# Kernel tuning notes

Hardware: AMD Instinct MI355X
Metric: run time of the kernel (lower is better)

The kernel has to match this reference:

```python
import jax, jax.numpy as jnp
import numpy as np

N, T, D, H = 64, 1024, 512, 512

def setup_inputs() -> dict:
    key = jax.random.key(0)
    k1, k2, k3, k4 = jax.random.split(key, 4)
    x = jax.random.normal(k1, (N, T, D), dtype=jnp.float32)
    h0 = jax.random.normal(k2, (N, H), dtype=jnp.float32)
    Wx = jax.random.normal(k3, (D, H), dtype=jnp.float32) / jnp.sqrt(jnp.float32(D))
    Wh = jax.random.normal(k4, (H, H), dtype=jnp.float32) / jnp.sqrt(jnp.float32(H))
    b = jnp.zeros((H,), dtype=jnp.float32)
    return {"x": x, "h0": h0, "Wx": Wx, "Wh": Wh, "b": b}

def reference(x, h0, Wx, Wh, b):
    # Precompute input projection for all timesteps: (N,T,H)
    xW = jnp.einsum('ntd,dh->nth', x, Wx) + b
    # Sequential recurrence over time via lax.scan
    def step(prev_h, xw_t):
        next_h = jnp.tanh(prev_h @ Wh + xw_t)  # (N,H)
        return next_h, next_h
    # scan over time axis: move T to leading axis
    _, h_seq = jax.lax.scan(step, h0, jnp.swapaxes(xW, 0, 1))  # (T,N,H)
    return jnp.swapaxes(h_seq, 0, 1)  # (N,T,H)
```

## Files before the change

### kernel.cpp

```cpp
#include <hip/hip_runtime.h>
#include <hip/hip_fp16.h>
#include <cstddef>
#include <cstdint>

#define NB 64
#define TT 1024
#define DD 512
#define HH 512

typedef _Float16 h2_t __attribute__((ext_vector_type(2)));
typedef __attribute__((ext_vector_type(8))) short bf16x8;
typedef __attribute__((ext_vector_type(4))) float f32x4;
typedef __attribute__((ext_vector_type(8))) unsigned short ushort8;

__device__ __forceinline__ float dot2f(uint32_t a, uint32_t b, float c) {
#if __has_builtin(__builtin_amdgcn_fdot2)
    return __builtin_amdgcn_fdot2(__builtin_bit_cast(h2_t, a),
                                  __builtin_bit_cast(h2_t, b), c, false);
#else
    __half2 av = __builtin_bit_cast(__half2, a);
    __half2 bv = __builtin_bit_cast(__half2, b);
    float2 af = __half22float2(av), bf = __half22float2(bv);
    return fmaf(af.x, bf.x, fmaf(af.y, bf.y, c));
#endif
}

__device__ __forceinline__ float fast_tanh(float z) {
    z = fmaxf(-15.f, fminf(15.f, z));
    float u = __builtin_amdgcn_exp2f(-2.885390082f * z);
    return (1.f - u) * __builtin_amdgcn_rcpf(1.f + u);
}

__device__ __forceinline__ unsigned short f2bf(float f) {
    uint32_t u = __builtin_bit_cast(uint32_t, f);
    u += 0x7FFFu + ((u >> 16) & 1u);
    return (unsigned short)(u >> 16);
}

__global__ void conv_x(const float* __restrict__ x,
                       unsigned short* __restrict__ xb, long total) {
    long i0 = (long)(blockIdx.x * blockDim.x + threadIdx.x) * 8;
    long stride = (long)gridDim.x * blockDim.x * 8;
    for (long i = i0; i < total; i += stride) {
        float4 a = *reinterpret_cast<const float4*>(&x[i]);
        float4 b = *reinterpret_cast<const float4*>(&x[i + 4]);
        ushort8 o;
        o[0] = f2bf(a.x); o[1] = f2bf(a.y); o[2] = f2bf(a.z); o[3] = f2bf(a.w);
        o[4] = f2bf(b.x); o[5] = f2bf(b.y); o[6] = f2bf(b.z); o[7] = f2bf(b.w);
        *reinterpret_cast<ushort8*>(&xb[i]) = o;
    }
}

__global__ void conv_wt(const float* __restrict__ W,
                        unsigned short* __restrict__ Wt) {
    int n = blockIdx.x;
    int kc = threadIdx.x;
    ushort8 o;
#pragma unroll
    for (int i = 0; i < 8; ++i)
        o[i] = f2bf(W[(size_t)(kc * 8 + i) * HH + n]);
    *reinterpret_cast<ushort8*>(&Wt[(size_t)n * DD + kc * 8]) = o;
}

#define GBM 128
#define GBN 128
#define GBK 64
#define LDSW 72

__global__ __launch_bounds__(256, 4) void gemm_bf16(
    const unsigned short* __restrict__ A,
    const unsigned short* __restrict__ Bt,
    const float* __restrict__ bias,
    float* __restrict__ C)
{
    __shared__ unsigned short As[GBM * LDSW];
    __shared__ unsigned short Bs[GBN * LDSW];

    const int tid  = threadIdx.x;
    const int m0   = blockIdx.x * GBM;
    const int n0   = blockIdx.y * GBN;
    const int lane = tid & 63;
    const int wave = tid >> 6;
    const int wm   = wave >> 1;
    const int wn   = wave & 1;

    const int srow = tid >> 3;
    const int sch  = tid & 7;

    f32x4 acc[4][4] = {};

    const int arow = wm * 64 + (lane & 15);
    const int brow = wn * 64 + (lane & 15);
    const int koff = (lane >> 4) * 8;

    for (int kt = 0; kt < DD / GBK; ++kt) {
        const int k0 = kt * GBK;
#pragma unroll
        for (int p = 0; p < 4; ++p) {
            const int row = srow + p * 32;
            *reinterpret_cast<ushort8*>(&As[row * LDSW + sch * 8]) =
                *reinterpret_cast<const ushort8*>(
                    &A[(size_t)(m0 + row) * DD + k0 + sch * 8]);
            *reinterpret_cast<ushort8*>(&Bs[row * LDSW + sch * 8]) =
                *reinterpret_cast<const ushort8*>(
                    &Bt[(size_t)(n0 + row) * DD + k0 + sch * 8]);
        }
        __syncthreads();

#pragma unroll
        for (int kk = 0; kk < GBK; kk += 32) {
            bf16x8 af[4], bf[4];
#pragma unroll
            for (int mt = 0; mt < 4; ++mt)
                af[mt] = *reinterpret_cast<const bf16x8*>(
                    &As[(arow + mt * 16) * LDSW + kk + koff]);
#pragma unroll
            for (int nt = 0; nt < 4; ++nt)
                bf[nt] = *reinterpret_cast<const bf16x8*>(
                    &Bs[(brow + nt * 16) * LDSW + kk + koff]);
#pragma unroll
            for (int mt = 0; mt < 4; ++mt)
#pragma unroll
                for (int nt = 0; nt < 4; ++nt)
                    acc[mt][nt] = __builtin_amdgcn_mfma_f32_16x16x32_bf16(
                        af[mt], bf[nt], acc[mt][nt], 0, 0, 0);
        }
        __syncthreads();
    }

#pragma unroll
    for (int nt = 0; nt < 4; ++nt) {
        const int col = n0 + wn * 64 + nt * 16 + (lane & 15);
        const float bv = bias[col];
#pragma unroll
        for (int mt = 0; mt < 4; ++mt) {
            const int rbase = m0 + wm * 64 + mt * 16 + (lane >> 4) * 4;
#pragma unroll
            for (int r = 0; r < 4; ++r)
                C[(size_t)(rbase + r) * HH + col] = acc[mt][nt][r] + bv;
        }
    }
}

#define BM 128
#define BN 128
#define BK 8

__global__ __launch_bounds__(256, 2) void gemm_xw(
    const float* __restrict__ A,
    const float* __restrict__ B,
    const float* __restrict__ bias,
    float* __restrict__ C)
{
    __shared__ float As[BK][BM];
    __shared__ float Bs[BK][BN];

    const int tid  = threadIdx.x;
    const int tm   = tid >> 4;
    const int tn   = tid & 15;
    const int row0 = blockIdx.x * BM;
    const int col0 = blockIdx.y * BN;

    const int ar = tid >> 1;
    const int ac = (tid & 1) * 4;
    const int br = tid >> 5;
    const int bc = (tid & 31) * 4;

    float acc[8][8];
#pragma unroll
    for (int i = 0; i < 8; ++i)
#pragma unroll
        for (int j = 0; j < 8; ++j) acc[i][j] = 0.f;

    for (int k0 = 0; k0 < DD; k0 += BK) {
        float4 av = *reinterpret_cast<const float4*>(
            &A[(size_t)(row0 + ar) * DD + k0 + ac]);
        float4 bv = *reinterpret_cast<const float4*>(
            &B[(size_t)(k0 + br) * HH + col0 + bc]);

        As[ac + 0][ar] = av.x;
        As[ac + 1][ar] = av.y;
        As[ac + 2][ar] = av.z;
        As[ac + 3][ar] = av.w;
        *reinterpret_cast<float4*>(&Bs[br][bc]) = bv;
        __syncthreads();

#pragma unroll
        for (int kk = 0; kk < BK; ++kk) {
            float a[8], b[8];
            *reinterpret_cast<float4*>(&a[0]) =
                *reinterpret_cast<const float4*>(&As[kk][tm * 8]);
            *reinterpret_cast<float4*>(&a[4]) =
                *reinterpret_cast<const float4*>(&As[kk][tm * 8 + 4]);
            *reinterpret_cast<float4*>(&b[0]) =
                *reinterpret_cast<const float4*>(&Bs[kk][tn * 8]);
            *reinterpret_cast<float4*>(&b[4]) =
                *reinterpret_cast<const float4*>(&Bs[kk][tn * 8 + 4]);
#pragma unroll
            for (int i = 0; i < 8; ++i)
#pragma unroll
                for (int j = 0; j < 8; ++j)
                    acc[i][j] = fmaf(a[i], b[j], acc[i][j]);
        }
        __syncthreads();
    }

#pragma unroll
    for (int i = 0; i < 8; ++i) {
        const int row = row0 + tm * 8 + i;
#pragma unroll
        for (int j = 0; j < 8; j += 4) {
            const int col = col0 + tn * 8 + j;
            float4 o;
            o.x = acc[i][j + 0] + bias[col + 0];
            o.y = acc[i][j + 1] + bias[col + 1];
            o.z = acc[i][j + 2] + bias[col + 2];
            o.w = acc[i][j + 3] + bias[col + 3];
            *reinterpret_cast<float4*>(&C[(size_t)row * HH + col]) = o;
        }
    }
}

__global__ __launch_bounds__(1024, 4) void rnn_scan_pkt(
    const float* __restrict__ Wh,
    const float* __restrict__ h0,
    float* __restrict__ out,
    uint64_t* __restrict__ exch)
{
    __shared__ __align__(16) uint32_t hp[2][HH / 2];
    __shared__ float partial[16][128];

    const int blk = blockIdx.x;
    const int x = blk & 7;
    const int i = blk >> 3;
    const int n = x + ((i & 7) << 3);
    const int r = i >> 3;
    const int jb = r << 7;

    const int tid = threadIdx.x;
    const int w = tid >> 6;
    const int l = tid & 63;

    uint32_t w0[16], w1[16];
    {
        const float* wc = Wh + (size_t)(w * 32) * HH + jb + l;
#pragma unroll
        for (int p = 0; p < 16; ++p) {
            float e0 = wc[(size_t)(2 * p) * HH];
            float e1 = wc[(size_t)(2 * p + 1) * HH];
            w0[p] = __builtin_bit_cast(uint32_t, __floats2half2_rn(e0, e1));
            float f0 = wc[(size_t)(2 * p) * HH + 64];
            float f1 = wc[(size_t)(2 * p + 1) * HH + 64];
            w1[p] = __builtin_bit_cast(uint32_t, __floats2half2_rn(f0, f1));
        }
    }

    if (tid < HH)
        ((__half*)hp[0])[tid] = __float2half(h0[(size_t)n * HH + tid]);
    __syncthreads();

    float* outn = out + (size_t)n * TT * HH;
    uint64_t* ex = exch + (size_t)n * 2 * HH;

    const int rcol = (jb + 128 + (tid - 128)) & (HH - 1);

    int cur = 0;
    for (int t = 0; t < TT; ++t) {
        const uint32_t T = (uint32_t)(t + 1);
        const int slot = (int)(T & 1u);

        float xw_r = 0.f;
        if (tid < 128) xw_r = outn[(size_t)t * HH + jb + tid];

        const uint32_t* hpw = &hp[cur][w * 16];
        float a0 = 0.f, a1 = 0.f, b0 = 0.f, b1 = 0.f;
#pragma unroll
        for (int q = 0; q < 4; ++q) {
            uint4 hv = ((const uint4*)hpw)[q];
            a0 = dot2f(hv.x, w0[4 * q + 0], a0);
            b0 = dot2f(hv.x, w1[4 * q + 0], b0);
            a1 = dot2f(hv.y, w0[4 * q + 1], a1);
            b1 = dot2f(hv.y, w1[4 * q + 1], b1);
            a0 = dot2f(hv.z, w0[4 * q + 2], a0);
            b0 = dot2f(hv.z, w1[4 * q + 2], b0);
            a1 = dot2f(hv.w, w0[4 * q + 3], a1);
            b1 = dot2f(hv.w, w1[4 * q + 3], b1);
        }
        partial[w][l] = a0 + a1;
        partial[w][64 + l] = b0 + b1;
        __syncthreads();

        __half* hpn = (__half*)hp[cur ^ 1];
        if (tid < 128) {
            float s = 0.f;
#pragma unroll
            for (int ww = 0; ww < 16; ++ww) s += partial[ww][tid];
            float h = fast_tanh(s + xw_r);
            outn[(size_t)t * HH + jb + tid] = h;
            hpn[jb + tid] = __float2half(h);
            uint64_t pk = ((uint64_t)T << 32) |
                          (uint64_t)__builtin_bit_cast(uint32_t, h);
            __hip_atomic_store(&ex[slot * HH + jb + tid], pk,
                               __ATOMIC_RELAXED, __HIP_MEMORY_SCOPE_AGENT);
        } else if (tid < 512) {
            uint64_t pk = __hip_atomic_load(&ex[slot * HH + rcol],
                                            __ATOMIC_RELAXED,
                                            __HIP_MEMORY_SCOPE_AGENT);
            while ((uint32_t)(pk >> 32) != T) {
                __builtin_amdgcn_s_sleep(1);
                pk = __hip_atomic_load(&ex[slot * HH + rcol],
                                       __ATOMIC_RELAXED,
                                       __HIP_MEMORY_SCOPE_AGENT);
            }
            hpn[rcol] = __float2half(__builtin_bit_cast(float, (uint32_t)pk));
        }
        __syncthreads();
        cur ^= 1;
    }
}

__global__ __launch_bounds__(512, 2) void rnn_scan_f32(
    const float* __restrict__ Wh,
    const float* __restrict__ h0,
    float* __restrict__ out)
{
    __shared__ float hbuf[2][HH];
    const int n = blockIdx.x;
    const int j = threadIdx.x;

    hbuf[0][j] = h0[(size_t)n * HH + j];
    __syncthreads();

    float* outn = out + (size_t)n * TT * HH;
    const float* __restrict__ wp = Wh + j;

    int cur = 0;
    for (int t = 0; t < TT; ++t) {
        float acc = outn[(size_t)t * HH + j];
        const float* hc = hbuf[cur];
#pragma unroll 4
        for (int k = 0; k < HH; k += 4) {
            float4 hv = *reinterpret_cast<const float4*>(&hc[k]);
            acc = fmaf(hv.x, wp[(size_t)(k + 0) * HH], acc);
            acc = fmaf(hv.y, wp[(size_t)(k + 1) * HH], acc);
            acc = fmaf(hv.z, wp[(size_t)(k + 2) * HH], acc);
            acc = fmaf(hv.w, wp[(size_t)(k + 3) * HH], acc);
        }
        float hn = tanhf(acc);
        outn[(size_t)t * HH + j] = hn;
        hbuf[cur ^ 1][j] = hn;
        cur ^= 1;
        __syncthreads();
    }
}

extern "C" void kernel_launch(void* const* d_in, const int* in_sizes, int n_in,
                              void* d_out, int out_size, void* d_ws, size_t ws_size,
                              hipStream_t stream) {
    const float* x  = (const float*)d_in[0];
    const float* h0 = (const float*)d_in[1];
    const float* Wx = (const float*)d_in[2];
    const float* Wh = (const float*)d_in[3];
    const float* b  = (const float*)d_in[4];
    float* out = (float*)d_out;

    const long   M        = (long)NB * TT;
    const size_t exch_b   = (size_t)NB * 2 * HH * 8;
    const size_t wt_b     = (size_t)HH * DD * 2;
    const size_t xb_b     = (size_t)M * DD * 2;
    const size_t need_mid = exch_b;
    const size_t need_all = exch_b + wt_b + xb_b;

    if (ws_size >= need_all) {
        uint64_t*       exch = (uint64_t*)d_ws;
        unsigned short* Wt   = (unsigned short*)((char*)d_ws + exch_b);
        unsigned short* xb   = (unsigned short*)((char*)d_ws + exch_b + wt_b);

        conv_x<<<2048, 256, 0, stream>>>(x, xb, M * DD);
        conv_wt<<<HH, 64, 0, stream>>>(Wx, Wt);
        dim3 gg(M / GBM, HH / GBN);
        gemm_bf16<<<gg, 256, 0, stream>>>(xb, Wt, b, out);
        rnn_scan_pkt<<<256, 1024, 0, stream>>>(Wh, h0, out, exch);
    } else if (ws_size >= need_mid) {
        dim3 g1(M / BM, HH / BN);
        gemm_xw<<<g1, 256, 0, stream>>>(x, Wx, b, out);
        rnn_scan_pkt<<<256, 1024, 0, stream>>>(Wh, h0, out, (uint64_t*)d_ws);
    } else {
        dim3 g1(M / BM, HH / BN);
        gemm_xw<<<g1, 256, 0, stream>>>(x, Wx, b, out);
        rnn_scan_f32<<<NB, 512, 0, stream>>>(Wh, h0, out);
    }
}
```

Measured before the change: 1.471 ms.

## Fuse bf16 conversion into GEMM and run recurrence in one block per sequence

```diff
diff --git a/kernel.cpp b/kernel.cpp
--- a/kernel.cpp
+++ b/kernel.cpp
@@ -7,6 +7,8 @@
 #define TT 1024
 #define DD 512
 #define HH 512
+#define WREG 92
+#define WLDS 36
 
 typedef _Float16 h2_t __attribute__((ext_vector_type(2)));
 typedef __attribute__((ext_vector_type(8))) short bf16x8;
@@ -37,20 +39,6 @@
     return (unsigned short)(u >> 16);
 }
 
-__global__ void conv_x(const float* __restrict__ x,
-                       unsigned short* __restrict__ xb, long total) {
-    long i0 = (long)(blockIdx.x * blockDim.x + threadIdx.x) * 8;
-    long stride = (long)gridDim.x * blockDim.x * 8;
-    for (long i = i0; i < total; i += stride) {
-        float4 a = *reinterpret_cast<const float4*>(&x[i]);
-        float4 b = *reinterpret_cast<const float4*>(&x[i + 4]);
-        ushort8 o;
-        o[0] = f2bf(a.x); o[1] = f2bf(a.y); o[2] = f2bf(a.z); o[3] = f2bf(a.w);
-        o[4] = f2bf(b.x); o[5] = f2bf(b.y); o[6] = f2bf(b.z); o[7] = f2bf(b.w);
-        *reinterpret_cast<ushort8*>(&xb[i]) = o;
-    }
-}
-
 __global__ void conv_wt(const float* __restrict__ W,
                         unsigned short* __restrict__ Wt) {
     int n = blockIdx.x;
@@ -67,8 +55,8 @@
 #define GBK 64
 #define LDSW 72
 
-__global__ __launch_bounds__(256, 4) void gemm_bf16(
-    const unsigned short* __restrict__ A,
+__global__ __launch_bounds__(256, 4) void gemm_bf16f(
+    const float* __restrict__ X,
     const unsigned short* __restrict__ Bt,
     const float* __restrict__ bias,
     float* __restrict__ C)
@@ -84,6 +72,8 @@
     const int wm   = wave >> 1;
     const int wn   = wave & 1;
 
+    const int axr = tid >> 1;
+    const int axc = (tid & 1) * 32;
     const int srow = tid >> 3;
     const int sch  = tid & 7;
 
@@ -95,12 +85,23 @@
 
     for (int kt = 0; kt < DD / GBK; ++kt) {
         const int k0 = kt * GBK;
+        {
+            const float* xp = &X[(size_t)(m0 + axr) * DD + k0 + axc];
+#pragma unroll
+            for (int i = 0; i < 4; ++i) {
+                float4 a = *reinterpret_cast<const float4*>(&xp[i * 8]);
+                float4 b = *reinterpret_cast<const float4*>(&xp[i * 8 + 4]);
+                ushort8 o;
+                o[0] = f2bf(a.x); o[1] = f2bf(a.y);
+                o[2] = f2bf(a.z); o[3] = f2bf(a.w);
+                o[4] = f2bf(b.x); o[5] = f2bf(b.y);
+                o[6] = f2bf(b.z); o[7] = f2bf(b.w);
+                *reinterpret_cast<ushort8*>(&As[axr * LDSW + axc + i * 8]) = o;
+            }
+        }
 #pragma unroll
         for (int p = 0; p < 4; ++p) {
             const int row = srow + p * 32;
-            *reinterpret_cast<ushort8*>(&As[row * LDSW + sch * 8]) =
-                *reinterpret_cast<const ushort8*>(
-                    &A[(size_t)(m0 + row) * DD + k0 + sch * 8]);
             *reinterpret_cast<ushort8*>(&Bs[row * LDSW + sch * 8]) =
                 *reinterpret_cast<const ushort8*>(
                     &Bt[(size_t)(n0 + row) * DD + k0 + sch * 8]);
@@ -221,136 +222,84 @@
     }
 }
 
-__global__ __launch_bounds__(1024, 4) void rnn_scan_pkt(
-    const float* __restrict__ Wh,
-    const float* __restrict__ h0,
-    float* __restrict__ out,
-    uint64_t* __restrict__ exch)
-{
-    __shared__ __align__(16) uint32_t hp[2][HH / 2];
-    __shared__ float partial[16][128];
-
-    const int blk = blockIdx.x;
-    const int x = blk & 7;
-    const int i = blk >> 3;
-    const int n = x + ((i & 7) << 3);
-    const int r = i >> 3;
-    const int jb = r << 7;
-
-    const int tid = threadIdx.x;
-    const int w = tid >> 6;
-    const int l = tid & 63;
-
-    uint32_t w0[16], w1[16];
-    {
-        const float* wc = Wh + (size_t)(w * 32) * HH + jb + l;
-#pragma unroll
-        for (int p = 0; p < 16; ++p) {
-            float e0 = wc[(size_t)(2 * p) * HH];
-            float e1 = wc[(size_t)(2 * p + 1) * HH];
-            w0[p] = __builtin_bit_cast(uint32_t, __floats2half2_rn(e0, e1));
-            float f0 = wc[(size_t)(2 * p) * HH + 64];
-            float f1 = wc[(size_t)(2 * p + 1) * HH + 64];
-            w1[p] = __builtin_bit_cast(uint32_t, __floats2half2_rn(f0, f1));
-        }
-    }
-
-    if (tid < HH)
-        ((__half*)hp[0])[tid] = __float2half(h0[(size_t)n * HH + tid]);
-    __syncthreads();
-
-    float* outn = out + (size_t)n * TT * HH;
-    uint64_t* ex = exch + (size_t)n * 2 * HH;
-
-    const int rcol = (jb + 128 + (tid - 128)) & (HH - 1);
-
-    int cur = 0;
-    for (int t = 0; t < TT; ++t) {
-        const uint32_t T = (uint32_t)(t + 1);
-        const int slot = (int)(T & 1u);
-
-        float xw_r = 0.f;
-        if (tid < 128) xw_r = outn[(size_t)t * HH + jb + tid];
-
-        const uint32_t* hpw = &hp[cur][w * 16];
-        float a0 = 0.f, a1 = 0.f, b0 = 0.f, b1 = 0.f;
-#pragma unroll
-        for (int q = 0; q < 4; ++q) {
-            uint4 hv = ((const uint4*)hpw)[q];
-            a0 = dot2f(hv.x, w0[4 * q + 0], a0);
-            b0 = dot2f(hv.x, w1[4 * q + 0], b0);
-            a1 = dot2f(hv.y, w0[4 * q + 1], a1);
-            b1 = dot2f(hv.y, w1[4 * q + 1], b1);
-            a0 = dot2f(hv.z, w0[4 * q + 2], a0);
-            b0 = dot2f(hv.z, w1[4 * q + 2], b0);
-            a1 = dot2f(hv.w, w0[4 * q + 3], a1);
-            b1 = dot2f(hv.w, w1[4 * q + 3], b1);
-        }
-        partial[w][l] = a0 + a1;
-        partial[w][64 + l] = b0 + b1;
-        __syncthreads();
-
-        __half* hpn = (__half*)hp[cur ^ 1];
-        if (tid < 128) {
-            float s = 0.f;
-#pragma unroll
-            for (int ww = 0; ww < 16; ++ww) s += partial[ww][tid];
-            float h = fast_tanh(s + xw_r);
-            outn[(size_t)t * HH + jb + tid] = h;
-            hpn[jb + tid] = __float2half(h);
-            uint64_t pk = ((uint64_t)T << 32) |
-                          (uint64_t)__builtin_bit_cast(uint32_t, h);
-            __hip_atomic_store(&ex[slot * HH + jb + tid], pk,
-                               __ATOMIC_RELAXED, __HIP_MEMORY_SCOPE_AGENT);
-        } else if (tid < 512) {
-            uint64_t pk = __hip_atomic_load(&ex[slot * HH + rcol],
-                                            __ATOMIC_RELAXED,
-                                            __HIP_MEMORY_SCOPE_AGENT);
-            while ((uint32_t)(pk >> 32) != T) {
-                __builtin_amdgcn_s_sleep(1);
-                pk = __hip_atomic_load(&ex[slot * HH + rcol],
-                                       __ATOMIC_RELAXED,
-                                       __HIP_MEMORY_SCOPE_AGENT);
-            }
-            hpn[rcol] = __float2half(__builtin_bit_cast(float, (uint32_t)pk));
-        }
-        __syncthreads();
-        cur ^= 1;
-    }
-}
-
-__global__ __launch_bounds__(512, 2) void rnn_scan_f32(
+__global__ __launch_bounds__(1024, 4) void rnn_scan_reg(
     const float* __restrict__ Wh,
     const float* __restrict__ h0,
     float* __restrict__ out)
 {
-    __shared__ float hbuf[2][HH];
-    const int n = blockIdx.x;
-    const int j = threadIdx.x;
-
-    hbuf[0][j] = h0[(size_t)n * HH + j];
+    __shared__ uint32_t Wl[2][9][HH][4];
+    __shared__ __align__(16) uint32_t hp[2][HH / 2];
+    __shared__ float partial[2][HH];
+
+    const int tid  = threadIdx.x;
+    const int j    = tid & (HH - 1);
+    const int half = tid >> 9;
+    const int n    = blockIdx.x;
+
+    uint32_t w[WREG];
+    {
+        const float* wc = Wh + (size_t)(half * 256) * HH + j;
+#pragma unroll
+        for (int p = 0; p < WREG; ++p) {
+            float e0 = wc[(size_t)(2 * p) * HH];
+            float e1 = wc[(size_t)(2 * p + 1) * HH];
+            w[p] = __builtin_bit_cast(uint32_t, __floats2half2_rn(e0, e1));
+        }
+    }
+    for (int idx = tid; idx < 2 * 9 * 4 * HH; idx += 1024) {
+        int jj  = idx & (HH - 1);
+        int e   = (idx >> 9) & 3;
+        int rem = idx >> 11;
+        int lg  = rem % 9;
+        int hf  = rem / 9;
+        int k2  = hf * 128 + WREG + 4 * lg + e;
+        float e0 = Wh[(size_t)(2 * k2) * HH + jj];
+        float e1 = Wh[(size_t)(2 * k2 + 1) * HH + jj];
+        Wl[hf][lg][jj][e] =
+            __builtin_bit_cast(uint32_t, __floats2half2_rn(e0, e1));
+    }
+
+    if (tid < HH)
+        ((__half*)hp[0])[tid] = __float2half(h0[(size_t)n * HH + tid]);
     __syncthreads();
 
     float* outn = out + (size_t)n * TT * HH;
-    const float* __restrict__ wp = Wh + j;
 
     int cur = 0;
     for (int t = 0; t < TT; ++t) {
-        float acc = outn[(size_t)t * HH + j];
-        const float* hc = hbuf[cur];
-#pragma unroll 4
-        for (int k = 0; k < HH; k += 4) {
-            float4 hv = *reinterpret_cast<const float4*>(&hc[k]);
-            acc = fmaf(hv.x, wp[(size_t)(k + 0) * HH], acc);
-            acc = fmaf(hv.y, wp[(size_t)(k + 1) * HH], acc);
-            acc = fmaf(hv.z, wp[(size_t)(k + 2) * HH], acc);
-            acc = fmaf(hv.w, wp[(size_t)(k + 3) * HH], acc);
-        }
-        float hn = tanhf(acc);
-        outn[(size_t)t * HH + j] = hn;
-        hbuf[cur ^ 1][j] = hn;
+        float xw = 0.f;
+        if (tid < HH) xw = outn[(size_t)t * HH + tid];
+
+        const uint4* hpw = (const uint4*)&hp[cur][half * 128];
+        float a0 = 0.f, a1 = 0.f, a2 = 0.f, a3 = 0.f;
+#pragma unroll
+        for (int q = 0; q < 23; ++q) {
+            uint4 hv = hpw[q];
+            a0 = dot2f(hv.x, w[4 * q + 0], a0);
+            a1 = dot2f(hv.y, w[4 * q + 1], a1);
+            a2 = dot2f(hv.z, w[4 * q + 2], a2);
+            a3 = dot2f(hv.w, w[4 * q + 3], a3);
+        }
+#pragma unroll
+        for (int lg = 0; lg < 9; ++lg) {
+            uint4 hv = hpw[23 + lg];
+            uint4 wl = *(const uint4*)&Wl[half][lg][j][0];
+            a0 = dot2f(hv.x, wl.x, a0);
+            a1 = dot2f(hv.y, wl.y, a1);
+            a2 = dot2f(hv.z, wl.z, a2);
+            a3 = dot2f(hv.w, wl.w, a3);
+        }
+        partial[half][j] = (a0 + a1) + (a2 + a3);
+        __syncthreads();
+
+        if (tid < HH) {
+            float z = partial[0][tid] + partial[1][tid] + xw;
+            float h = fast_tanh(z);
+            outn[(size_t)t * HH + tid] = h;
+            ((__half*)hp[cur ^ 1])[tid] = __float2half(h);
+        }
+        __syncthreads();
         cur ^= 1;
-        __syncthreads();
     }
 }
 
@@ -364,30 +313,17 @@
     const float* b  = (const float*)d_in[4];
     float* out = (float*)d_out;
 
-    const long   M        = (long)NB * TT;
-    const size_t exch_b   = (size_t)NB * 2 * HH * 8;
-    const size_t wt_b     = (size_t)HH * DD * 2;
-    const size_t xb_b     = (size_t)M * DD * 2;
-    const size_t need_mid = exch_b;
-    const size_t need_all = exch_b + wt_b + xb_b;
-
-    if (ws_size >= need_all) {
-        uint64_t*       exch = (uint64_t*)d_ws;
-        unsigned short* Wt   = (unsigned short*)((char*)d_ws + exch_b);
-        unsigned short* xb   = (unsigned short*)((char*)d_ws + exch_b + wt_b);
-
-        conv_x<<<2048, 256, 0, stream>>>(x, xb, M * DD);
+    const long   M    = (long)NB * TT;
+    const size_t wt_b = (size_t)HH * DD * 2;
+
+    if (ws_size >= wt_b) {
+        unsigned short* Wt = (unsigned short*)d_ws;
         conv_wt<<<HH, 64, 0, stream>>>(Wx, Wt);
         dim3 gg(M / GBM, HH / GBN);
-        gemm_bf16<<<gg, 256, 0, stream>>>(xb, Wt, b, out);
-        rnn_scan_pkt<<<256, 1024, 0, stream>>>(Wh, h0, out, exch);
-    } else if (ws_size >= need_mid) {
-        dim3 g1(M / BM, HH / BN);
-        gemm_xw<<<g1, 256, 0, stream>>>(x, Wx, b, out);
-        rnn_scan_pkt<<<256, 1024, 0, stream>>>(Wh, h0, out, (uint64_t*)d_ws);
+        gemm_bf16f<<<gg, 256, 0, stream>>>(x, Wt, b, out);
     } else {
         dim3 g1(M / BM, HH / BN);
         gemm_xw<<<g1, 256, 0, stream>>>(x, Wx, b, out);
-        rnn_scan_f32<<<NB, 512, 0, stream>>>(Wh, h0, out);
-    }
-}
+    }
+    rnn_scan_reg<<<NB, 1024, 0, stream>>>(Wh, h0, out);
+}
```

Result: slower. 1.862 ms (+26.6%).
